# Performance work log

Measured on AMD Instinct MI355X. Metric: run time of the kernel, lower is better.

Reference implementation:

```python
import jax, jax.numpy as jnp
import numpy as np

D_MODEL = 1024
NUM_HEADS = 16
HEAD_DIM = D_MODEL // NUM_HEADS
SCALE = HEAD_DIM ** -0.5


def setup_inputs() -> dict:
    key = jax.random.key(0)
    k1, k2, k3 = jax.random.split(key, 3)
    x = jax.random.normal(k1, (4, 2048, D_MODEL), dtype=jnp.float32)
    # torch Linear stores weight [out, in]; we store transposed [in, out] for x @ W
    w_qkv = jax.random.normal(k2, (D_MODEL, 3 * D_MODEL), dtype=jnp.float32) * (D_MODEL ** -0.5)
    w_out = jax.random.normal(k3, (D_MODEL, D_MODEL), dtype=jnp.float32) * (D_MODEL ** -0.5)
    return {"x": x, "w_qkv": w_qkv, "w_out": w_out}


def reference(x, w_qkv, w_out):
    batch, seq_len, _ = x.shape
    qkv = x @ w_qkv  # [B, S, 3*D]
    q, k, v = jnp.split(qkv, 3, axis=-1)

    def to_heads(t):
        return t.reshape(batch, seq_len, NUM_HEADS, HEAD_DIM).transpose(0, 2, 1, 3)  # [B, H, S, Dh]

    q, k, v = to_heads(q), to_heads(k), to_heads(v)
    attn = jnp.einsum('bhqd,bhkd->bhqk', q, k) * SCALE  # [B, H, S, S]
    causal = jnp.tril(jnp.ones((seq_len, seq_len), dtype=bool))
    attn = jnp.where(causal[None, None], attn, -jnp.inf)
    attn = jax.nn.softmax(attn, axis=-1)
    out = jnp.einsum('bhqk,bhkd->bhqd', attn, v)  # [B, H, S, Dh]
    out = out.transpose(0, 2, 1, 3).reshape(batch, seq_len, D_MODEL)
    return out @ w_out
```

## Files before the change

kernel.cpp:

```cpp
#include <hip/hip_runtime.h>
#include <hip/hip_bf16.h>

typedef unsigned short u16;
typedef float f32x4 __attribute__((ext_vector_type(4)));
typedef __bf16 bf16x8 __attribute__((ext_vector_type(8)));
typedef u16 u16x8 __attribute__((ext_vector_type(8)));
typedef u16 u16x4 __attribute__((ext_vector_type(4)));
typedef unsigned u32x2 __attribute__((ext_vector_type(2)));

__device__ __forceinline__ u16 f2bf(float f) {
  unsigned u = __builtin_bit_cast(unsigned, f);
  u = (u + 0x7fffu + ((u >> 16) & 1u)) >> 16;
  return (u16)u;
}

__device__ __forceinline__ unsigned cvtpk(float lo, float hi) {
  unsigned r;
  asm("v_cvt_pk_bf16_f32 %0, %1, %2" : "=v"(r) : "v"(lo), "v"(hi));
  return r;
}

__device__ __forceinline__ float exp2b(float x) {
  return __builtin_amdgcn_exp2f(x);
}

__device__ __forceinline__ void gload16(const void* g, void* l) {
  __builtin_amdgcn_global_load_lds(
      (const __attribute__((address_space(1))) unsigned*)g,
      (__attribute__((address_space(3))) unsigned*)l, 16, 0, 0);
}

__device__ __forceinline__ f32x4 mfma16(bf16x8 a, bf16x8 b, f32x4 c) {
  return __builtin_amdgcn_mfma_f32_16x16x32_bf16(a, b, c, 0, 0, 0);
}

__global__ __launch_bounds__(256) void convx(const float4* __restrict__ x,
                                             u16x8* __restrict__ xb, int n) {
  int i = blockIdx.x * 256 + threadIdx.x;
  if (i >= n) return;
  float4 a = x[2 * i], b = x[2 * i + 1];
  u16x8 o;
  o[0] = f2bf(a.x); o[1] = f2bf(a.y); o[2] = f2bf(a.z); o[3] = f2bf(a.w);
  o[4] = f2bf(b.x); o[5] = f2bf(b.y); o[6] = f2bf(b.z); o[7] = f2bf(b.w);
  xb[i] = o;
}

__global__ __launch_bounds__(256) void transpose_w(const float* __restrict__ w,
                                                   u16* __restrict__ wt,
                                                   int R, int C) {
  __shared__ float tile[32][33];
  int n0 = blockIdx.x * 32, k0 = blockIdx.y * 32;
  int tx = threadIdx.x & 31, ty = threadIdx.x >> 5;
#pragma unroll
  for (int j = 0; j < 32; j += 8)
    tile[ty + j][tx] = w[(size_t)(k0 + ty + j) * C + n0 + tx];
  __syncthreads();
#pragma unroll
  for (int j = 0; j < 32; j += 8)
    wt[(size_t)(n0 + ty + j) * R + k0 + tx] = f2bf(tile[tx][ty + j]);
}

template <int MODE, int BM, int BN, int WGM, int WGN>
__global__ __launch_bounds__(512, 2) void gemm_t(const u16* __restrict__ A,
                                                 const u16* __restrict__ Bt,
                                                 void* __restrict__ Cv,
                                                 int M, int N, int K,
                                                 u16* __restrict__ Qb,
                                                 u16* __restrict__ Kb) {
  constexpr int PWM = BM / WGM, PWN = BN / WGN;
  constexpr int MI = PWM / 16, MH = MI / 2;
  static_assert(PWN == 64, "per-wave N must be 64 (NI=4)");
  constexpr int ALD = BM / 128, BLD = BN / 128, LPT = ALD + BLD;
  __shared__ alignas(16) u16 As[4][BM][32];
  __shared__ alignas(16) u16 Bs[4][BN][32];
  const int tix = threadIdx.x;
  const int lane = tix & 63, wid = tix >> 6;
  const int wm = wid / WGN, wn = wid % WGN;
  const int r = lane & 15, g = lane >> 4;
  const int s2 = (r >> 1) & 3;
  const int m0 = blockIdx.y * BM, n0 = blockIdx.x * BN;

  const int srow = tix >> 2;
  const int swc = (tix & 3) ^ ((srow >> 1) & 3);
  const u16* gA[ALD];
  const u16* gB[BLD];
#pragma unroll
  for (int i = 0; i < ALD; ++i)
    gA[i] = A + (size_t)(m0 + i * 128 + srow) * K + swc * 8;
#pragma unroll
  for (int i = 0; i < BLD; ++i)
    gB[i] = Bt + (size_t)(n0 + i * 128 + srow) * K + swc * 8;

  auto SA = [&](int tt) {
    const int ko = tt * 32, bu_ = tt & 3;
#pragma unroll
    for (int i = 0; i < ALD; ++i)
      gload16(gA[i] + ko, &As[bu_][i * 128 + wid * 16][0]);
  };
  auto SB = [&](int tt) {
    const int ko = tt * 32, bu_ = tt & 3;
#pragma unroll
    for (int i = 0; i < BLD; ++i)
      gload16(gB[i] + ko, &Bs[bu_][i * 128 + wid * 16][0]);
  };

  f32x4 acc[MI][4] = {};
  const int NT = K >> 5;

  SA(0); SB(0); SA(1); SB(1); SA(2); SB(2);

  for (int t = 0; t < NT; ++t) {
    if (t < NT - 2) {
      if constexpr (LPT == 4) asm volatile("s_waitcnt vmcnt(8)" ::: "memory");
      else                    asm volatile("s_waitcnt vmcnt(6)" ::: "memory");
    } else if (t == NT - 2) {
      if constexpr (LPT == 4) asm volatile("s_waitcnt vmcnt(4)" ::: "memory");
      else                    asm volatile("s_waitcnt vmcnt(3)" ::: "memory");
    } else {
      asm volatile("s_waitcnt vmcnt(0)" ::: "memory");
    }
    __builtin_amdgcn_s_barrier();
    __builtin_amdgcn_sched_barrier(0);

    const int bu = t & 3;
    bf16x8 a0[MH], bf[4];
#pragma unroll
    for (int mi = 0; mi < MH; ++mi)
      a0[mi] = *(const bf16x8*)&As[bu][wm * PWM + mi * 16 + r][(g ^ s2) * 8];
#pragma unroll
    for (int ni = 0; ni < 4; ++ni)
      bf[ni] = *(const bf16x8*)&Bs[bu][wn * 64 + ni * 16 + r][(g ^ s2) * 8];
    if (t + 3 < NT) SA(t + 3);
    __builtin_amdgcn_s_barrier();
    asm volatile("s_waitcnt lgkmcnt(0)" ::: "memory");
    __builtin_amdgcn_sched_barrier(0);
    __builtin_amdgcn_s_setprio(1);
#pragma unroll
    for (int mi = 0; mi < MH; ++mi)
#pragma unroll
      for (int ni = 0; ni < 4; ++ni)
        acc[mi][ni] = mfma16(a0[mi], bf[ni], acc[mi][ni]);
    __builtin_amdgcn_s_setprio(0);
    __builtin_amdgcn_s_barrier();

    bf16x8 a1[MH];
#pragma unroll
    for (int mi = 0; mi < MH; ++mi)
      a1[mi] = *(const bf16x8*)&As[bu][wm * PWM + (MH + mi) * 16 + r][(g ^ s2) * 8];
    if (t + 3 < NT) SB(t + 3);
    __builtin_amdgcn_s_barrier();
    asm volatile("s_waitcnt lgkmcnt(0)" ::: "memory");
    __builtin_amdgcn_sched_barrier(0);
    __builtin_amdgcn_s_setprio(1);
#pragma unroll
    for (int mi = 0; mi < MH; ++mi)
#pragma unroll
      for (int ni = 0; ni < 4; ++ni)
        acc[MH + mi][ni] = mfma16(a1[mi], bf[ni], acc[MH + mi][ni]);
    __builtin_amdgcn_s_setprio(0);
  }

#pragma unroll
  for (int mi = 0; mi < MI; ++mi) {
    int row = m0 + wm * PWM + mi * 16 + g * 4;
#pragma unroll
    for (int ni = 0; ni < 4; ++ni) {
      int col = n0 + wn * 64 + ni * 16 + r;
#pragma unroll
      for (int e = 0; e < 4; ++e) {
        float v = acc[mi][ni][e];
        int rr = row + e;
        if (MODE == 0) {
          ((u16*)Cv)[(size_t)rr * N + col] = f2bf(v);
        } else if (MODE == 2) {
          ((float*)Cv)[(size_t)rr * N + col] = v;
        } else {
          int which = col >> 10, hh = (col >> 6) & 15, dd = col & 63;
          int bb = rr >> 11, ss = rr & 2047;
          size_t idx = ((size_t)(bb * 16 + hh) * 2048 + ss) * 64 + dd;
          (which ? Kb : Qb)[idx] = f2bf(which ? v : v * 0.18033688011112042f);
        }
      }
    }
  }
}

__global__ __launch_bounds__(512, 6) void attn_fwd(const u16* __restrict__ Q,
                                                   const u16* __restrict__ Kc,
                                                   const u16* __restrict__ Vt,
                                                   u16* __restrict__ O) {
  __shared__ alignas(16) u16 Ks[2][64][64];
  __shared__ alignas(16) u16 Vs[2][64][64];
  __shared__ alignas(16) u16 Ps[8][16][72];
  const int lane = threadIdx.x & 63, wid = threadIdx.x >> 6;
  const int r = lane & 15, g = lane >> 4;
  const int bh = blockIdx.x, b = bh >> 4, h = bh & 15;
  const int qb = 15 - (int)blockIdx.y;
  const int qw = qb * 128 + wid * 16;
  const int nkv = 2 * (qb + 1);

  const u16* Kp = Kc + (size_t)bh * 2048 * 64;
  const u16* Vp = Vt + (size_t)(h * 64) * 8192 + (size_t)b * 2048;
  const u16* Qp = Q + ((size_t)bh * 2048 + qw) * 64;
  u16* pw = &Ps[wid][0][0];

  const int srow = lane >> 3;
  const int scol = ((lane & 7) ^ srow) * 8;

  bf16x8 qf[2];
  qf[0] = *(const bf16x8*)(Qp + (size_t)r * 64 + g * 8);
  qf[1] = *(const bf16x8*)(Qp + (size_t)r * 64 + 32 + g * 8);

  u16x8 ov8;
#pragma unroll
  for (int i = 0; i < 8; ++i) ov8[i] = 0x3F80;
  const bf16x8 ones = __builtin_bit_cast(bf16x8, ov8);

  f32x4 o[5] = {};

  gload16(Kp + (size_t)(wid * 8 + srow) * 64 + scol, &Ks[0][wid * 8][0]);
  gload16(Vp + (size_t)(wid * 8 + srow) * 8192 + scol, &Vs[0][wid * 8][0]);

  int cur = 0;
  for (int t = 0; t < nkv; ++t, cur ^= 1) {
    __syncthreads();
    if (t + 1 < nkv) {
      const int kn = (t + 1) * 64;
      gload16(Kp + (size_t)(kn + wid * 8 + srow) * 64 + scol, &Ks[cur ^ 1][wid * 8][0]);
      gload16(Vp + (size_t)(wid * 8 + srow) * 8192 + kn + scol, &Vs[cur ^ 1][wid * 8][0]);
    }
    const int kv0 = t * 64;
    if (kv0 > qw + 15) continue;

    f32x4 s[4];
    __builtin_amdgcn_s_setprio(1);
#pragma unroll
    for (int tt = 0; tt < 4; ++tt) {
      bf16x8 k0 = *(const bf16x8*)&Ks[cur][tt * 16 + r][((0 + g) ^ (r & 7)) * 8];
      bf16x8 k1 = *(const bf16x8*)&Ks[cur][tt * 16 + r][((4 + g) ^ (r & 7)) * 8];
      f32x4 z = {-16.f, -16.f, -16.f, -16.f};
      z = mfma16(k0, qf[0], z);
      z = mfma16(k1, qf[1], z);
      s[tt] = z;
    }
    __builtin_amdgcn_s_setprio(0);
    if (kv0 + 63 > qw) {
#pragma unroll
      for (int tt = 0; tt < 4; ++tt) {
        int kvb = kv0 + tt * 16 + g * 4;
#pragma unroll
        for (int e = 0; e < 4; ++e)
          if (kvb + e > qw + r) s[tt][e] = -1e30f;
      }
    }

#pragma unroll
    for (int tt = 0; tt < 4; ++tt) {
      float p0 = exp2b(s[tt][0]), p1 = exp2b(s[tt][1]);
      float p2 = exp2b(s[tt][2]), p3 = exp2b(s[tt][3]);
      u32x2 w;
      w[0] = cvtpk(p0, p1);
      w[1] = cvtpk(p2, p3);
      *(u32x2*)&pw[r * 72 + tt * 16 + g * 4] = w;
    }

    bf16x8 pB0 = *(const bf16x8*)&pw[r * 72 + g * 8];
    bf16x8 pB1 = *(const bf16x8*)&pw[r * 72 + 32 + g * 8];
    __builtin_amdgcn_s_setprio(1);
#pragma unroll
    for (int dt = 0; dt < 4; ++dt) {
      bf16x8 v0 = *(const bf16x8*)&Vs[cur][dt * 16 + r][((0 + g) ^ (r & 7)) * 8];
      bf16x8 v1 = *(const bf16x8*)&Vs[cur][dt * 16 + r][((4 + g) ^ (r & 7)) * 8];
      o[dt] = mfma16(v0, pB0, o[dt]);
      o[dt] = mfma16(v1, pB1, o[dt]);
    }
    o[4] = mfma16(ones, pB0, o[4]);
    o[4] = mfma16(ones, pB1, o[4]);
    __builtin_amdgcn_s_setprio(0);
  }

  float inv = 1.f / o[4][0];
  size_t rowbase = ((size_t)b * 2048 + qw + r) * 1024 + h * 64;
#pragma unroll
  for (int dt = 0; dt < 4; ++dt) {
    u16x4 ov;
#pragma unroll
    for (int e = 0; e < 4; ++e) ov[e] = f2bf(o[dt][e] * inv);
    *(u16x4*)&O[rowbase + dt * 16 + g * 4] = ov;
  }
}

extern "C" void kernel_launch(void* const* d_in, const int* in_sizes, int n_in,
                              void* d_out, int out_size, void* d_ws,
                              size_t ws_size, hipStream_t stream) {
  const float* x = (const float*)d_in[0];
  const float* wqkv = (const float*)d_in[1];
  const float* wout = (const float*)d_in[2];
  float* out = (float*)d_out;
  char* ws = (char*)d_ws;

  u16* Xb = (u16*)ws;
  u16* Wt = (u16*)(ws + (16ull << 20));
  u16* WoT = (u16*)(ws + (22ull << 20));
  u16* Qb = (u16*)(ws + (24ull << 20));
  u16* Kb = (u16*)(ws + (40ull << 20));
  u16* Vt = (u16*)(ws + (56ull << 20));

  convx<<<4096, 256, 0, stream>>>((const float4*)x, (u16x8*)Xb, 1048576);
  transpose_w<<<dim3(96, 32), 256, 0, stream>>>(wqkv, Wt, 1024, 3072);
  transpose_w<<<dim3(32, 32), 256, 0, stream>>>(wout, WoT, 1024, 1024);

  gemm_t<1, 256, 256, 2, 4><<<dim3(8, 32), 512, 0, stream>>>(
      Xb, Wt, nullptr, 8192, 2048, 1024, Qb, Kb);
  gemm_t<0, 128, 256, 2, 4><<<dim3(32, 8), 512, 0, stream>>>(
      Wt + (size_t)2048 * 1024, Xb, Vt, 1024, 8192, 1024, nullptr, nullptr);
  attn_fwd<<<dim3(64, 16), 512, 0, stream>>>(Qb, Kb, Vt, Xb);
  gemm_t<2, 256, 128, 4, 2><<<dim3(8, 32), 512, 0, stream>>>(
      Xb, WoT, out, 8192, 1024, 1024, nullptr, nullptr);
}
```

Before: 168.2 us.

## Shrink GEMM tiles and LDS ring to three stages for higher occupancy

Reduces the GEMM shared-memory ring from four to three stages, prefetching two tiles ahead, and adds a single-phase MFMA path for small per-wave M. The three projection GEMMs switch to smaller tiles (256x128 or 128x128) with higher waves-per-EU launch bounds, giving more blocks and more resident workgroups per CU. The aim is better CU utilisation and latency hiding through occupancy, at the cost of less data reuse per tile and a shallower prefetch pipeline.

New measurement: 155.3 us, median of 2. 7.7% less time.

```diff
diff --git a/kernel.cpp b/kernel.cpp
--- a/kernel.cpp
+++ b/kernel.cpp
@@ -60,19 +60,21 @@
     wt[(size_t)(n0 + ty + j) * R + k0 + tx] = f2bf(tile[tx][ty + j]);
 }
 
-template <int MODE, int BM, int BN, int WGM, int WGN>
-__global__ __launch_bounds__(512, 2) void gemm_t(const u16* __restrict__ A,
-                                                 const u16* __restrict__ Bt,
-                                                 void* __restrict__ Cv,
-                                                 int M, int N, int K,
-                                                 u16* __restrict__ Qb,
-                                                 u16* __restrict__ Kb) {
+template <int MODE, int BM, int BN, int WGM, int WGN, int WPE>
+__global__ __launch_bounds__(512, WPE) void gemm_t(const u16* __restrict__ A,
+                                                   const u16* __restrict__ Bt,
+                                                   void* __restrict__ Cv,
+                                                   int M, int N, int K,
+                                                   u16* __restrict__ Qb,
+                                                   u16* __restrict__ Kb) {
   constexpr int PWM = BM / WGM, PWN = BN / WGN;
-  constexpr int MI = PWM / 16, MH = MI / 2;
+  constexpr int MI = PWM / 16;
+  constexpr bool PH2 = (MI >= 4);
+  constexpr int MH = PH2 ? MI / 2 : MI;
   static_assert(PWN == 64, "per-wave N must be 64 (NI=4)");
   constexpr int ALD = BM / 128, BLD = BN / 128, LPT = ALD + BLD;
-  __shared__ alignas(16) u16 As[4][BM][32];
-  __shared__ alignas(16) u16 Bs[4][BN][32];
+  __shared__ alignas(16) u16 As[3][BM][32];
+  __shared__ alignas(16) u16 Bs[3][BN][32];
   const int tix = threadIdx.x;
   const int lane = tix & 63, wid = tix >> 6;
   const int wm = wid / WGN, wn = wid % WGN;
@@ -91,38 +93,37 @@
   for (int i = 0; i < BLD; ++i)
     gB[i] = Bt + (size_t)(n0 + i * 128 + srow) * K + swc * 8;
 
-  auto SA = [&](int tt) {
-    const int ko = tt * 32, bu_ = tt & 3;
+  auto SA = [&](int tt, int bb) {
+    const int ko = tt * 32;
 #pragma unroll
     for (int i = 0; i < ALD; ++i)
-      gload16(gA[i] + ko, &As[bu_][i * 128 + wid * 16][0]);
+      gload16(gA[i] + ko, &As[bb][i * 128 + wid * 16][0]);
   };
-  auto SB = [&](int tt) {
-    const int ko = tt * 32, bu_ = tt & 3;
+  auto SB = [&](int tt, int bb) {
+    const int ko = tt * 32;
 #pragma unroll
     for (int i = 0; i < BLD; ++i)
-      gload16(gB[i] + ko, &Bs[bu_][i * 128 + wid * 16][0]);
+      gload16(gB[i] + ko, &Bs[bb][i * 128 + wid * 16][0]);
   };
 
   f32x4 acc[MI][4] = {};
   const int NT = K >> 5;
 
-  SA(0); SB(0); SA(1); SB(1); SA(2); SB(2);
-
+  SA(0, 0); SB(0, 0); SA(1, 1); SB(1, 1);
+
+  int bu = 0;
   for (int t = 0; t < NT; ++t) {
-    if (t < NT - 2) {
-      if constexpr (LPT == 4) asm volatile("s_waitcnt vmcnt(8)" ::: "memory");
-      else                    asm volatile("s_waitcnt vmcnt(6)" ::: "memory");
-    } else if (t == NT - 2) {
-      if constexpr (LPT == 4) asm volatile("s_waitcnt vmcnt(4)" ::: "memory");
-      else                    asm volatile("s_waitcnt vmcnt(3)" ::: "memory");
+    if (t < NT - 1) {
+      if constexpr (LPT == 3) asm volatile("s_waitcnt vmcnt(3)" ::: "memory");
+      else                    asm volatile("s_waitcnt vmcnt(2)" ::: "memory");
     } else {
       asm volatile("s_waitcnt vmcnt(0)" ::: "memory");
     }
     __builtin_amdgcn_s_barrier();
     __builtin_amdgcn_sched_barrier(0);
 
-    const int bu = t & 3;
+    const int bs = (bu >= 1) ? bu - 1 : 2;
+
     bf16x8 a0[MH], bf[4];
 #pragma unroll
     for (int mi = 0; mi < MH; ++mi)
@@ -130,34 +131,50 @@
 #pragma unroll
     for (int ni = 0; ni < 4; ++ni)
       bf[ni] = *(const bf16x8*)&Bs[bu][wn * 64 + ni * 16 + r][(g ^ s2) * 8];
-    if (t + 3 < NT) SA(t + 3);
-    __builtin_amdgcn_s_barrier();
-    asm volatile("s_waitcnt lgkmcnt(0)" ::: "memory");
-    __builtin_amdgcn_sched_barrier(0);
-    __builtin_amdgcn_s_setprio(1);
-#pragma unroll
-    for (int mi = 0; mi < MH; ++mi)
-#pragma unroll
-      for (int ni = 0; ni < 4; ++ni)
-        acc[mi][ni] = mfma16(a0[mi], bf[ni], acc[mi][ni]);
-    __builtin_amdgcn_s_setprio(0);
-    __builtin_amdgcn_s_barrier();
-
-    bf16x8 a1[MH];
-#pragma unroll
-    for (int mi = 0; mi < MH; ++mi)
-      a1[mi] = *(const bf16x8*)&As[bu][wm * PWM + (MH + mi) * 16 + r][(g ^ s2) * 8];
-    if (t + 3 < NT) SB(t + 3);
-    __builtin_amdgcn_s_barrier();
-    asm volatile("s_waitcnt lgkmcnt(0)" ::: "memory");
-    __builtin_amdgcn_sched_barrier(0);
-    __builtin_amdgcn_s_setprio(1);
-#pragma unroll
-    for (int mi = 0; mi < MH; ++mi)
-#pragma unroll
-      for (int ni = 0; ni < 4; ++ni)
-        acc[MH + mi][ni] = mfma16(a1[mi], bf[ni], acc[MH + mi][ni]);
-    __builtin_amdgcn_s_setprio(0);
+    if (t + 2 < NT) SA(t + 2, bs);
+
+    if constexpr (PH2) {
+      __builtin_amdgcn_s_barrier();
+      asm volatile("s_waitcnt lgkmcnt(0)" ::: "memory");
+      __builtin_amdgcn_sched_barrier(0);
+      __builtin_amdgcn_s_setprio(1);
+#pragma unroll
+      for (int mi = 0; mi < MH; ++mi)
+#pragma unroll
+        for (int ni = 0; ni < 4; ++ni)
+          acc[mi][ni] = mfma16(a0[mi], bf[ni], acc[mi][ni]);
+      __builtin_amdgcn_s_setprio(0);
+      __builtin_amdgcn_s_barrier();
+
+      bf16x8 a1[MH];
+#pragma unroll
+      for (int mi = 0; mi < MH; ++mi)
+        a1[mi] = *(const bf16x8*)&As[bu][wm * PWM + (MH + mi) * 16 + r][(g ^ s2) * 8];
+      if (t + 2 < NT) SB(t + 2, bs);
+      __builtin_amdgcn_s_barrier();
+      asm volatile("s_waitcnt lgkmcnt(0)" ::: "memory");
+      __builtin_amdgcn_sched_barrier(0);
+      __builtin_amdgcn_s_setprio(1);
+#pragma unroll
+      for (int mi = 0; mi < MH; ++mi)
+#pragma unroll
+        for (int ni = 0; ni < 4; ++ni)
+          acc[MH + mi][ni] = mfma16(a1[mi], bf[ni], acc[MH + mi][ni]);
+      __builtin_amdgcn_s_setprio(0);
+    } else {
+      if (t + 2 < NT) SB(t + 2, bs);
+      __builtin_amdgcn_s_barrier();
+      asm volatile("s_waitcnt lgkmcnt(0)" ::: "memory");
+      __builtin_amdgcn_sched_barrier(0);
+      __builtin_amdgcn_s_setprio(1);
+#pragma unroll
+      for (int mi = 0; mi < MI; ++mi)
+#pragma unroll
+        for (int ni = 0; ni < 4; ++ni)
+          acc[mi][ni] = mfma16(a0[mi], bf[ni], acc[mi][ni]);
+      __builtin_amdgcn_s_setprio(0);
+    }
+    bu = (bu + 1 >= 3) ? 0 : bu + 1;
   }
 
 #pragma unroll
@@ -310,11 +327,11 @@
   transpose_w<<<dim3(96, 32), 256, 0, stream>>>(wqkv, Wt, 1024, 3072);
   transpose_w<<<dim3(32, 32), 256, 0, stream>>>(wout, WoT, 1024, 1024);
 
-  gemm_t<1, 256, 256, 2, 4><<<dim3(8, 32), 512, 0, stream>>>(
+  gemm_t<1, 256, 128, 4, 2, 4><<<dim3(16, 32), 512, 0, stream>>>(
       Xb, Wt, nullptr, 8192, 2048, 1024, Qb, Kb);
-  gemm_t<0, 128, 256, 2, 4><<<dim3(32, 8), 512, 0, stream>>>(
+  gemm_t<0, 128, 128, 4, 2, 6><<<dim3(64, 8), 512, 0, stream>>>(
       Wt + (size_t)2048 * 1024, Xb, Vt, 1024, 8192, 1024, nullptr, nullptr);
   attn_fwd<<<dim3(64, 16), 512, 0, stream>>>(Qb, Kb, Vt, Xb);
-  gemm_t<2, 256, 128, 4, 2><<<dim3(8, 32), 512, 0, stream>>>(
+  gemm_t<2, 128, 128, 4, 2, 6><<<dim3(8, 64), 512, 0, stream>>>(
       Xb, WoT, out, 8192, 1024, 1024, nullptr, nullptr);
 }
```
